# Optimization experiments

Hardware: AMD Instinct MI355X
Metric: run time of the kernel (lower is better)

The kernel has to match this reference:

```python
import jax, jax.numpy as jnp
import numpy as np


def setup_inputs() -> dict:
    key = jax.random.key(0)
    k1, k2 = jax.random.split(key)
    # x: (B, C, D, H, W); w: (out_ch, C * 2*2*2)
    x = jax.random.normal(k1, (4, 64, 33, 33, 33), dtype=jnp.float32)
    w = jax.random.normal(k2, (128, 64 * 8), dtype=jnp.float32) * 0.05
    return {"x": x, "w": w}


def reference(x, w):
    # unfoldNd(kernel=2, stride=1, pad=0) + einsum('ij,kjm->kim', w, patches)
    # is exactly a valid 3D cross-correlation with a 2x2x2 kernel.
    B, C, D, H, W = x.shape
    O = w.shape[0]
    kern = w.reshape(O, C, 2, 2, 2)  # unfold flattening order: (C, kd, kh, kw)
    y = jax.lax.conv_general_dilated(
        x, kern,
        window_strides=(1, 1, 1),
        padding='VALID',
        dimension_numbers=('NCDHW', 'OIDHW', 'NCDHW'),
    )  # (B, O, D-1, H-1, W-1)
    return (y + 1.0) ** 2
```

## Files before the change

### kernel.cpp

```cpp
#include <hip/hip_runtime.h>

typedef __bf16 bf16x8 __attribute__((ext_vector_type(8)));
typedef float f32x4 __attribute__((ext_vector_type(4)));
typedef unsigned short u16;
typedef unsigned int u32;
typedef u32 u32x4 __attribute__((ext_vector_type(4)));
typedef u16 u16x8 __attribute__((ext_vector_type(8)));

#define AS1 __attribute__((address_space(1)))
#define AS3 __attribute__((address_space(3)))
#define GLL16(gp, lp) __builtin_amdgcn_global_load_lds((const AS1 void*)(gp), (AS3 void*)(lp), 16, 0, 0)
#define GLL4(gp, lp)  __builtin_amdgcn_global_load_lds((const AS1 void*)(gp), (AS3 void*)(lp), 4, 0, 0)

__device__ __forceinline__ u16 f32_to_bf16_rne(float f) {
    union { float f; unsigned u; } cv; cv.f = f;
    unsigned u = cv.u;
    return (u16)((u + 0x7FFFu + ((u >> 16) & 1u)) >> 16);
}

__device__ __forceinline__ u32 cvt_pk_bf16(float lo, float hi) {
    u32 r;
    asm("v_cvt_pk_bf16_f32 %0, %1, %2" : "=v"(r) : "v"(lo), "v"(hi));
    return r;
}

__global__ void repack_w_kernel(const float* __restrict__ w, u16* __restrict__ w3) {
    int e = blockIdx.x * 256 + threadIdx.x;
    int j    = e & 7;
    int g    = (e >> 3) & 3;
    int o    = (e >> 5) & 127;
    int cb   = (e >> 12) & 1;
    int koff = (e >> 13) & 7;
    int c = (cb << 5) + (g << 3) + j;
    w3[e] = f32_to_bf16_rne(w[(o << 9) + (c << 3) + koff]);
}

__global__ __launch_bounds__(256) void transpose_x_kernel(
    const float* __restrict__ x, u16* __restrict__ xT, u16* __restrict__ x32) {

    __shared__ float t[64][34];
    const int bid = blockIdx.x;
    const int h = bid % 33;
    const int dq = bid / 33;
    const int d = dq % 33;
    const int b = dq / 33;
    const float* xp = x + (size_t)b * 2299968 + d * 1089 + h * 33;

    const int tid = threadIdx.x;
    const int wv  = tid & 31;
    const int c0  = tid >> 5;
#pragma unroll
    for (int i = 0; i < 8; ++i) {
        int c = c0 + (i << 3);
        t[c][wv] = xp[(size_t)c * 35937 + wv];
    }
    if (tid < 64) t[tid][32] = xp[(size_t)tid * 35937 + 32];
    __syncthreads();

    const int cc = tid >> 5;
    u32x4 v;
    v[0] = cvt_pk_bf16(t[cc * 8 + 0][wv], t[cc * 8 + 1][wv]);
    v[1] = cvt_pk_bf16(t[cc * 8 + 2][wv], t[cc * 8 + 3][wv]);
    v[2] = cvt_pk_bf16(t[cc * 8 + 4][wv], t[cc * 8 + 5][wv]);
    v[3] = cvt_pk_bf16(t[cc * 8 + 6][wv], t[cc * 8 + 7][wv]);
    *reinterpret_cast<u32x4*>(&xT[(size_t)bid * 2048 + cc * 256 + wv * 8]) = v;

    if (tid < 8) {
        u32x4 m;
        m[0] = cvt_pk_bf16(t[tid * 8 + 0][32], t[tid * 8 + 1][32]);
        m[1] = cvt_pk_bf16(t[tid * 8 + 2][32], t[tid * 8 + 3][32]);
        m[2] = cvt_pk_bf16(t[tid * 8 + 4][32], t[tid * 8 + 5][32]);
        m[3] = cvt_pk_bf16(t[tid * 8 + 6][32], t[tid * 8 + 7][32]);
        *reinterpret_cast<u32x4*>(&x32[(size_t)bid * 64 + tid * 8]) = m;
    }
}

__global__ __launch_bounds__(256, 4) void conv_mfma_kernel(
    const u16* __restrict__ xT, const u16* __restrict__ x32,
    const u16* __restrict__ w3, float* __restrict__ out) {

    __shared__ __align__(16) u16 xs[12672];

    const int tid = threadIdx.x;
    const int bid = blockIdx.x;
    const int hy0 = (bid & 15) << 1;
    const int dz  = (bid >> 4) & 31;
    const int b   = bid >> 9;

    char* ldsb = (char*)xs;
    const int wave_off = (tid >> 6) << 10;
#pragma unroll
    for (int s = 0; s < 6; ++s) {
        const int kd = (s >= 3) ? 1 : 0;
        const int kh = s - kd * 3;
        const size_t gslab = (size_t)(b * 1089 + (dz + kd) * 33 + (hy0 + kh));
        const char* src = (const char*)xT + (gslab << 12) + (tid << 4);
        GLL16(src, ldsb + (s << 12) + wave_off + ((tid & 63) << 4));
    }
    if (tid < 192) {
        const int kd = tid / 96;
        const int r  = (tid << 2) - kd * 384;
        const char* src = (const char*)x32
            + ((size_t)(b * 1089 + (dz + kd) * 33 + hy0) << 7) + r;
        GLL4(src, ldsb + 24576 + ((tid >> 6) << 8) + ((tid & 63) << 2));
    }
    asm volatile("s_waitcnt vmcnt(0)" ::: "memory");
    __syncthreads();

    const int lane = tid & 63;
    const int ln   = lane & 15;
    const int g    = lane >> 4;
    const int n0w  = (tid >> 6) << 5;

    f32x4 acc[2][4];
#pragma unroll
    for (int nf = 0; nf < 2; ++nf)
#pragma unroll
        for (int mf = 0; mf < 4; ++mf)
            acc[nf][mf] = (f32x4){0.f, 0.f, 0.f, 0.f};

#pragma unroll
    for (int cb = 0; cb < 2; ++cb) {
        const int cc = (cb << 2) + g;
#pragma unroll
        for (int kd = 0; kd < 2; ++kd) {
            bf16x8 wf[2][4];
#pragma unroll
            for (int nf = 0; nf < 2; ++nf)
#pragma unroll
                for (int kk = 0; kk < 4; ++kk) {
                    const int koff = (kd << 2) + kk;
                    const u16* p = w3 + (size_t)((((koff << 1) + cb) << 7)
                                   + n0w + (nf << 4) + ln) * 32 + (g << 3);
                    wf[nf][kk] = __builtin_bit_cast(bf16x8, *reinterpret_cast<const u16x8*>(p));
                }
#pragma unroll
            for (int kw = 0; kw < 2; ++kw) {
                bf16x8 xf[3][2];
#pragma unroll
                for (int hh = 0; hh < 3; ++hh)
#pragma unroll
                    for (int wh = 0; wh < 2; ++wh) {
                        const int row = (wh << 4) + ln + kw;
                        const u16* p = (row < 32)
                            ? &xs[(((kd * 3 + hh) << 11)) + (cc << 8) + (row << 3)]
                            : &xs[12288 + kd * 192 + hh * 64 + (cc << 3)];
                        xf[hh][wh] = __builtin_bit_cast(bf16x8,
                            *reinterpret_cast<const u16x8*>(p));
                    }
#pragma unroll
                for (int kh = 0; kh < 2; ++kh)
#pragma unroll
                    for (int nf = 0; nf < 2; ++nf)
#pragma unroll
                        for (int mf = 0; mf < 4; ++mf)
                            acc[nf][mf] = __builtin_amdgcn_mfma_f32_16x16x32_bf16(
                                wf[nf][(kh << 1) + kw], xf[(mf >> 1) + kh][mf & 1],
                                acc[nf][mf], 0, 0, 0);
            }
        }
    }

    float* ob = out + ((size_t)b * 128) * 32768 + (dz << 10) + (hy0 << 5);
#pragma unroll
    for (int nf = 0; nf < 2; ++nf)
#pragma unroll
        for (int mf = 0; mf < 4; ++mf) {
            const int wx   = ((mf & 1) << 4) + ln;
            const int hrow = mf >> 1;
            float* o2 = ob + (hrow << 5) + wx;
#pragma unroll
            for (int r = 0; r < 4; ++r) {
                const int n = n0w + (nf << 4) + (g << 2) + r;
                float v = acc[nf][mf][r] + 1.0f;
                o2[(size_t)n << 15] = v * v;
            }
        }
}

#define XS_ROW 72
__global__ __launch_bounds__(256, 4) void conv_mfma_fallback(
    const float* __restrict__ x, const u16* __restrict__ w3, float* __restrict__ out) {

    __shared__ __align__(16) u16 xs[6 * 33 * XS_ROW];

    const int tid = threadIdx.x;
    const int bid = blockIdx.x;
    const int hy0 = (bid & 15) << 1;
    const int dz  = (bid >> 4) & 31;
    const int b   = bid >> 9;

    const float* xb = x + (size_t)b * 64 * 35937;
    for (int i = tid; i < 1584; i += 256) {
        int w   = i % 33;
        int t   = i / 33;
        int q   = t & 7;
        int kh3 = t >> 3;
        int kd  = kh3 >= 3 ? 1 : 0;
        int kh  = kh3 - kd * 3;
        const float* p = xb + (size_t)(q << 3) * 35937 + (dz + kd) * 1089 + (hy0 + kh) * 33 + w;
        u32x4 v;
        v[0] = cvt_pk_bf16(p[0], p[35937]);
        v[1] = cvt_pk_bf16(p[2 * 35937], p[3 * 35937]);
        v[2] = cvt_pk_bf16(p[4 * 35937], p[5 * 35937]);
        v[3] = cvt_pk_bf16(p[6 * 35937], p[7 * 35937]);
        *reinterpret_cast<u32x4*>(&xs[(kh3 * 33 + w) * XS_ROW + (q << 3)]) = v;
    }
    __syncthreads();

    const int lane = tid & 63;
    const int ln   = lane & 15;
    const int g    = lane >> 4;
    const int n0w  = (tid >> 6) << 5;

    f32x4 acc[2][4];
#pragma unroll
    for (int nf = 0; nf < 2; ++nf)
#pragma unroll
        for (int mf = 0; mf < 4; ++mf)
            acc[nf][mf] = (f32x4){0.f, 0.f, 0.f, 0.f};

#pragma unroll
    for (int cb = 0; cb < 2; ++cb) {
        const int cbase = (cb << 5) + (g << 3);
#pragma unroll
        for (int kd = 0; kd < 2; ++kd) {
            bf16x8 wf[2][4];
#pragma unroll
            for (int nf = 0; nf < 2; ++nf)
#pragma unroll
                for (int kk = 0; kk < 4; ++kk) {
                    const int koff = (kd << 2) + kk;
                    const u16* p = w3 + (size_t)((((koff << 1) + cb) << 7)
                                   + n0w + (nf << 4) + ln) * 32 + (g << 3);
                    wf[nf][kk] = __builtin_bit_cast(bf16x8, *reinterpret_cast<const u16x8*>(p));
                }
#pragma unroll
            for (int kw = 0; kw < 2; ++kw) {
                bf16x8 xf[3][2];
#pragma unroll
                for (int hh = 0; hh < 3; ++hh)
#pragma unroll
                    for (int wh = 0; wh < 2; ++wh) {
                        const int row = (kd * 3 + hh) * 33 + (wh << 4) + ln + kw;
                        xf[hh][wh] = __builtin_bit_cast(bf16x8,
                            *reinterpret_cast<const u16x8*>(&xs[row * XS_ROW + cbase]));
                    }
#pragma unroll
                for (int kh = 0; kh < 2; ++kh)
#pragma unroll
                    for (int nf = 0; nf < 2; ++nf)
#pragma unroll
                        for (int mf = 0; mf < 4; ++mf)
                            acc[nf][mf] = __builtin_amdgcn_mfma_f32_16x16x32_bf16(
                                wf[nf][(kh << 1) + kw], xf[(mf >> 1) + kh][mf & 1],
                                acc[nf][mf], 0, 0, 0);
            }
        }
    }

    float* ob = out + ((size_t)b * 128) * 32768 + (dz << 10) + (hy0 << 5);
#pragma unroll
    for (int nf = 0; nf < 2; ++nf)
#pragma unroll
        for (int mf = 0; mf < 4; ++mf) {
            const int wx   = ((mf & 1) << 4) + ln;
            const int hrow = mf >> 1;
            float* o2 = ob + (hrow << 5) + wx;
#pragma unroll
            for (int r = 0; r < 4; ++r) {
                const int n = n0w + (nf << 4) + (g << 2) + r;
                float v = acc[nf][mf][r] + 1.0f;
                o2[(size_t)n << 15] = v * v;
            }
        }
}

extern "C" void kernel_launch(void* const* d_in, const int* in_sizes, int n_in,
                              void* d_out, int out_size, void* d_ws, size_t ws_size,
                              hipStream_t stream) {
    const float* x = (const float*)d_in[0];
    const float* w = (const float*)d_in[1];
    float* out = (float*)d_out;

    const size_t W3_BYTES  = 131072;
    const size_t XT_BYTES  = (size_t)4356 * 4096;
    const size_t X32_BYTES = (size_t)4356 * 128;
    const size_t NEED = W3_BYTES + XT_BYTES + X32_BYTES;

    u16* w3 = (u16*)d_ws;
    repack_w_kernel<<<256, 256, 0, stream>>>(w, w3);

    if (ws_size >= NEED) {
        u16* xT  = (u16*)((char*)d_ws + W3_BYTES);
        u16* x32 = (u16*)((char*)d_ws + W3_BYTES + XT_BYTES);
        transpose_x_kernel<<<4356, 256, 0, stream>>>(x, xT, x32);
        conv_mfma_kernel<<<2048, 256, 0, stream>>>(xT, x32, w3, out);
    } else {
        conv_mfma_fallback<<<2048, 256, 0, stream>>>(x, w3, out);
    }
}
```

Measured before the change: 51.95 us.

## Compute two depth slices per block sharing input slabs; drop LDS transpose

The conv kernel now computes two output depth planes per block of 512 threads. It loads three depth slabs into LDS instead of two per plane, so the middle slab serves both planes, and each wave covers 16 output channels with two accumulator sets. This cuts redundant global-to-LDS input traffic and halves the grid. The transpose kernel also drops its shared-memory staging and has each thread read its 8 channels directly from global memory. That read pattern is strided and may coalesce less well.

```diff
diff --git a/kernel.cpp b/kernel.cpp
--- a/kernel.cpp
+++ b/kernel.cpp
@@ -10,7 +10,6 @@
 #define AS1 __attribute__((address_space(1)))
 #define AS3 __attribute__((address_space(3)))
 #define GLL16(gp, lp) __builtin_amdgcn_global_load_lds((const AS1 void*)(gp), (AS3 void*)(lp), 16, 0, 0)
-#define GLL4(gp, lp)  __builtin_amdgcn_global_load_lds((const AS1 void*)(gp), (AS3 void*)(lp), 4, 0, 0)
 
 __device__ __forceinline__ u16 f32_to_bf16_rne(float f) {
     union { float f; unsigned u; } cv; cv.f = f;
@@ -38,7 +37,6 @@
 __global__ __launch_bounds__(256) void transpose_x_kernel(
     const float* __restrict__ x, u16* __restrict__ xT, u16* __restrict__ x32) {
 
-    __shared__ float t[64][34];
     const int bid = blockIdx.x;
     const int h = bid % 33;
     const int dq = bid / 33;
@@ -48,61 +46,59 @@
 
     const int tid = threadIdx.x;
     const int wv  = tid & 31;
-    const int c0  = tid >> 5;
-#pragma unroll
-    for (int i = 0; i < 8; ++i) {
-        int c = c0 + (i << 3);
-        t[c][wv] = xp[(size_t)c * 35937 + wv];
-    }
-    if (tid < 64) t[tid][32] = xp[(size_t)tid * 35937 + 32];
-    __syncthreads();
-
-    const int cc = tid >> 5;
+    const int cc  = tid >> 5;
+    const float* p = xp + (size_t)cc * 8 * 35937 + wv;
+    float f0 = p[0],              f1 = p[35937],          f2 = p[2 * 35937], f3 = p[3 * 35937];
+    float f4 = p[(size_t)4*35937],f5 = p[(size_t)5*35937],f6 = p[(size_t)6*35937],f7 = p[(size_t)7*35937];
     u32x4 v;
-    v[0] = cvt_pk_bf16(t[cc * 8 + 0][wv], t[cc * 8 + 1][wv]);
-    v[1] = cvt_pk_bf16(t[cc * 8 + 2][wv], t[cc * 8 + 3][wv]);
-    v[2] = cvt_pk_bf16(t[cc * 8 + 4][wv], t[cc * 8 + 5][wv]);
-    v[3] = cvt_pk_bf16(t[cc * 8 + 6][wv], t[cc * 8 + 7][wv]);
+    v[0] = cvt_pk_bf16(f0, f1);
+    v[1] = cvt_pk_bf16(f2, f3);
+    v[2] = cvt_pk_bf16(f4, f5);
+    v[3] = cvt_pk_bf16(f6, f7);
     *reinterpret_cast<u32x4*>(&xT[(size_t)bid * 2048 + cc * 256 + wv * 8]) = v;
 
     if (tid < 8) {
+        const float* q = xp + (size_t)tid * 8 * 35937 + 32;
         u32x4 m;
-        m[0] = cvt_pk_bf16(t[tid * 8 + 0][32], t[tid * 8 + 1][32]);
-        m[1] = cvt_pk_bf16(t[tid * 8 + 2][32], t[tid * 8 + 3][32]);
-        m[2] = cvt_pk_bf16(t[tid * 8 + 4][32], t[tid * 8 + 5][32]);
-        m[3] = cvt_pk_bf16(t[tid * 8 + 6][32], t[tid * 8 + 7][32]);
+        m[0] = cvt_pk_bf16(q[0],              q[35937]);
+        m[1] = cvt_pk_bf16(q[2 * 35937],      q[3 * 35937]);
+        m[2] = cvt_pk_bf16(q[(size_t)4*35937],q[(size_t)5*35937]);
+        m[3] = cvt_pk_bf16(q[(size_t)6*35937],q[(size_t)7*35937]);
         *reinterpret_cast<u32x4*>(&x32[(size_t)bid * 64 + tid * 8]) = m;
     }
 }
 
-__global__ __launch_bounds__(256, 4) void conv_mfma_kernel(
+__global__ __launch_bounds__(512, 4) void conv_mfma_kernel(
     const u16* __restrict__ xT, const u16* __restrict__ x32,
     const u16* __restrict__ w3, float* __restrict__ out) {
 
-    __shared__ __align__(16) u16 xs[12672];
+    __shared__ __align__(16) u16 xs[19008];
 
     const int tid = threadIdx.x;
     const int bid = blockIdx.x;
     const int hy0 = (bid & 15) << 1;
-    const int dz  = (bid >> 4) & 31;
-    const int b   = bid >> 9;
+    const int dz0 = ((bid >> 4) & 15) << 1;
+    const int b   = bid >> 8;
 
     char* ldsb = (char*)xs;
-    const int wave_off = (tid >> 6) << 10;
-#pragma unroll
-    for (int s = 0; s < 6; ++s) {
-        const int kd = (s >= 3) ? 1 : 0;
-        const int kh = s - kd * 3;
-        const size_t gslab = (size_t)(b * 1089 + (dz + kd) * 33 + (hy0 + kh));
-        const char* src = (const char*)xT + (gslab << 12) + (tid << 4);
-        GLL16(src, ldsb + (s << 12) + wave_off + ((tid & 63) << 4));
-    }
-    if (tid < 192) {
-        const int kd = tid / 96;
-        const int r  = (tid << 2) - kd * 384;
+    const int slab0 = b * 1089 + dz0 * 33 + hy0;
+#pragma unroll
+    for (int r = 0; r < 5; ++r) {
+        if (r == 4 && tid >= 256) continue;
+        const int u   = tid + (r << 9);
+        const int sid = u >> 8;
+        const int s   = (sid * 171) >> 9;
+        const int hh  = sid - s * 3;
+        const char* src = (const char*)xT + ((size_t)(slab0 + s * 33 + hh) << 12)
+                          + ((u & 255) << 4);
+        GLL16(src, ldsb + (u << 4));
+    }
+    if (tid < 72) {
+        const int s  = (tid * 171) >> 12;
+        const int rr = tid - s * 24;
         const char* src = (const char*)x32
-            + ((size_t)(b * 1089 + (dz + kd) * 33 + hy0) << 7) + r;
-        GLL4(src, ldsb + 24576 + ((tid >> 6) << 8) + ((tid & 63) << 2));
+            + ((size_t)(b * 1089 + (dz0 + s) * 33 + hy0) << 7) + (rr << 4);
+        GLL16(src, ldsb + 36864 + (tid << 4));
     }
     asm volatile("s_waitcnt vmcnt(0)" ::: "memory");
     __syncthreads();
@@ -110,30 +106,33 @@
     const int lane = tid & 63;
     const int ln   = lane & 15;
     const int g    = lane >> 4;
-    const int n0w  = (tid >> 6) << 5;
-
-    f32x4 acc[2][4];
-#pragma unroll
-    for (int nf = 0; nf < 2; ++nf)
-#pragma unroll
-        for (int mf = 0; mf < 4; ++mf)
-            acc[nf][mf] = (f32x4){0.f, 0.f, 0.f, 0.f};
+    const int o0   = (tid >> 6) << 4;
+
+    f32x4 acc0[4], acc1[4];
+#pragma unroll
+    for (int mf = 0; mf < 4; ++mf) {
+        acc0[mf] = (f32x4){0.f, 0.f, 0.f, 0.f};
+        acc1[mf] = (f32x4){0.f, 0.f, 0.f, 0.f};
+    }
 
 #pragma unroll
     for (int cb = 0; cb < 2; ++cb) {
         const int cc = (cb << 2) + g;
-#pragma unroll
-        for (int kd = 0; kd < 2; ++kd) {
-            bf16x8 wf[2][4];
-#pragma unroll
-            for (int nf = 0; nf < 2; ++nf)
+        bf16x8 wfA[4], wfB[4];
+#pragma unroll
+        for (int kk = 0; kk < 4; ++kk) {
+            const u16* p = w3 + ((size_t)(((kk << 1) + cb) * 128 + o0 + ln) << 5) + (g << 3);
+            wfA[kk] = __builtin_bit_cast(bf16x8, *reinterpret_cast<const u16x8*>(p));
+        }
+#pragma unroll
+        for (int s = 0; s < 3; ++s) {
+            if (s == 1) {
 #pragma unroll
                 for (int kk = 0; kk < 4; ++kk) {
-                    const int koff = (kd << 2) + kk;
-                    const u16* p = w3 + (size_t)((((koff << 1) + cb) << 7)
-                                   + n0w + (nf << 4) + ln) * 32 + (g << 3);
-                    wf[nf][kk] = __builtin_bit_cast(bf16x8, *reinterpret_cast<const u16x8*>(p));
+                    const u16* p = w3 + ((size_t)((((4 + kk) << 1) + cb) * 128 + o0 + ln) << 5) + (g << 3);
+                    wfB[kk] = __builtin_bit_cast(bf16x8, *reinterpret_cast<const u16x8*>(p));
                 }
+            }
 #pragma unroll
             for (int kw = 0; kw < 2; ++kw) {
                 bf16x8 xf[3][2];
@@ -143,39 +142,44 @@
                     for (int wh = 0; wh < 2; ++wh) {
                         const int row = (wh << 4) + ln + kw;
                         const u16* p = (row < 32)
-                            ? &xs[(((kd * 3 + hh) << 11)) + (cc << 8) + (row << 3)]
-                            : &xs[12288 + kd * 192 + hh * 64 + (cc << 3)];
+                            ? &xs[((s * 3 + hh) << 11) + (cc << 8) + (row << 3)]
+                            : &xs[18432 + s * 192 + hh * 64 + (cc << 3)];
                         xf[hh][wh] = __builtin_bit_cast(bf16x8,
                             *reinterpret_cast<const u16x8*>(p));
                     }
 #pragma unroll
-                for (int kh = 0; kh < 2; ++kh)
-#pragma unroll
-                    for (int nf = 0; nf < 2; ++nf)
-#pragma unroll
-                        for (int mf = 0; mf < 4; ++mf)
-                            acc[nf][mf] = __builtin_amdgcn_mfma_f32_16x16x32_bf16(
-                                wf[nf][(kh << 1) + kw], xf[(mf >> 1) + kh][mf & 1],
-                                acc[nf][mf], 0, 0, 0);
+                for (int kh = 0; kh < 2; ++kh) {
+                    const int kk = (kh << 1) + kw;
+#pragma unroll
+                    for (int mf = 0; mf < 4; ++mf) {
+                        const bf16x8 xv = xf[(mf >> 1) + kh][mf & 1];
+                        if (s < 2)
+                            acc0[mf] = __builtin_amdgcn_mfma_f32_16x16x32_bf16(
+                                (s == 0 ? wfA : wfB)[kk], xv, acc0[mf], 0, 0, 0);
+                        if (s >= 1)
+                            acc1[mf] = __builtin_amdgcn_mfma_f32_16x16x32_bf16(
+                                (s == 1 ? wfA : wfB)[kk], xv, acc1[mf], 0, 0, 0);
+                    }
+                }
             }
         }
     }
 
-    float* ob = out + ((size_t)b * 128) * 32768 + (dz << 10) + (hy0 << 5);
-#pragma unroll
-    for (int nf = 0; nf < 2; ++nf)
-#pragma unroll
-        for (int mf = 0; mf < 4; ++mf) {
-            const int wx   = ((mf & 1) << 4) + ln;
-            const int hrow = mf >> 1;
-            float* o2 = ob + (hrow << 5) + wx;
-#pragma unroll
-            for (int r = 0; r < 4; ++r) {
-                const int n = n0w + (nf << 4) + (g << 2) + r;
-                float v = acc[nf][mf][r] + 1.0f;
-                o2[(size_t)n << 15] = v * v;
-            }
-        }
+    float* ob = out + (size_t)b * 128 * 32768 + ((size_t)dz0 << 10) + (hy0 << 5);
+#pragma unroll
+    for (int mf = 0; mf < 4; ++mf) {
+        const int wx   = ((mf & 1) << 4) + ln;
+        const int hrow = mf >> 1;
+#pragma unroll
+        for (int r = 0; r < 4; ++r) {
+            const int n = o0 + (g << 2) + r;
+            float* o2 = ob + ((size_t)n << 15) + (hrow << 5) + wx;
+            float v0 = acc0[mf][r] + 1.0f;
+            o2[0] = v0 * v0;
+            float v1 = acc1[mf][r] + 1.0f;
+            o2[1024] = v1 * v1;
+        }
+    }
 }
 
 #define XS_ROW 72
@@ -295,7 +299,7 @@
         u16* xT  = (u16*)((char*)d_ws + W3_BYTES);
         u16* x32 = (u16*)((char*)d_ws + W3_BYTES + XT_BYTES);
         transpose_x_kernel<<<4356, 256, 0, stream>>>(x, xT, x32);
-        conv_mfma_kernel<<<2048, 256, 0, stream>>>(xT, x32, w3, out);
+        conv_mfma_kernel<<<1024, 512, 0, stream>>>(xT, x32, w3, out);
     } else {
         conv_mfma_fallback<<<2048, 256, 0, stream>>>(x, w3, out);
     }
```

After: 47.31 us. 8.9% less time.
